# Optimization experiments

Measured on AMD Instinct MI355X. Metric: run time of the kernel, lower is better.

Reference implementation:

```python
import jax, jax.numpy as jnp
import numpy as np

N = 50000
E = 1000000
D_IN = 128
D_HID = 128
D_EMB = 128
D_DEG = 32
NEG_SLOPE = 0.2


def _add_self_loops(src, dst, n):
    loop = jnp.arange(n, dtype=src.dtype)
    return jnp.concatenate([src, loop]), jnp.concatenate([dst, loop])


def gat_conv(x, src, dst, W, a_src, a_dst, b, n):
    """PyG GATConv, heads=1, add_self_loops=True. src/dst already include self loops."""
    h = x @ W                                   # [n, d_out]
    hs = h[src]                                 # [e, d_out] gather (message sources)
    e = jax.nn.leaky_relu(hs @ a_src + h[dst] @ a_dst, NEG_SLOPE)  # [e]
    m = jax.ops.segment_max(e, dst, num_segments=n)
    e = jnp.exp(e - m[dst])
    denom = jax.ops.segment_sum(e, dst, num_segments=n)
    alpha = e / (denom[dst] + 1e-16)
    out = jax.ops.segment_sum(alpha[:, None] * hs, dst, num_segments=n)
    return out + b


def setup_inputs() -> dict:
    key = jax.random.key(0)
    ks = jax.random.split(key, 24)
    p = lambda k, shape: (jax.random.normal(k, shape, dtype=jnp.float32) * 0.05)
    inp = {
        "x_o": jax.random.normal(ks[0], (N, D_IN), dtype=jnp.float32),
        "degree_o": jax.random.normal(ks[1], (N, D_DEG), dtype=jnp.float32),
        "edge_index_o": jax.random.randint(ks[2], (2, E), 0, N, dtype=jnp.int32),
        "edge_index_s": jax.random.randint(ks[3], (2, E), 0, N, dtype=jnp.int32),
        # GAT layer params: o1, o2, s1, s2
        "W_o1": p(ks[4], (D_IN, D_HID)), "a_src_o1": p(ks[5], (D_HID,)), "a_dst_o1": p(ks[6], (D_HID,)), "b_o1": jnp.zeros((D_HID,), jnp.float32),
        "W_o2": p(ks[7], (D_HID, D_EMB)), "a_src_o2": p(ks[8], (D_EMB,)), "a_dst_o2": p(ks[9], (D_EMB,)), "b_o2": jnp.zeros((D_EMB,), jnp.float32),
        "W_s1": p(ks[10], (D_IN, D_HID)), "a_src_s1": p(ks[11], (D_HID,)), "a_dst_s1": p(ks[12], (D_HID,)), "b_s1": jnp.zeros((D_HID,), jnp.float32),
        "W_s2": p(ks[13], (D_HID, D_EMB)), "a_src_s2": p(ks[14], (D_EMB,)), "a_dst_s2": p(ks[15], (D_EMB,)), "b_s2": jnp.zeros((D_EMB,), jnp.float32),
        "W_pred": p(ks[16], (2 * D_EMB + D_DEG, 2)), "b_pred": jnp.zeros((2,), jnp.float32),
    }
    return inp


def reference(x_o, degree_o,
              W_o1, a_src_o1, a_dst_o1, b_o1,
              W_o2, a_src_o2, a_dst_o2, b_o2,
              W_s1, a_src_s1, a_dst_s1, b_s1,
              W_s2, a_src_s2, a_dst_s2, b_s2,
              W_pred, b_pred,
              edge_index_o, edge_index_s):
    n = x_o.shape[0]
    src_o, dst_o = _add_self_loops(edge_index_o[0], edge_index_o[1], n)
    src_s, dst_s = _add_self_loops(edge_index_s[0], edge_index_s[1], n)

    # branch o (original graph); dropout is identity in eval mode
    x1_o = jax.nn.relu(gat_conv(x_o, src_o, dst_o, W_o1, a_src_o1, a_dst_o1, b_o1, n))
    x2_o = gat_conv(x1_o, src_o, dst_o, W_o2, a_src_o2, a_dst_o2, b_o2, n)
    # branch s (second graph)
    x1_s = jax.nn.relu(gat_conv(x_o, src_s, dst_s, W_s1, a_src_s1, a_dst_s1, b_s1, n))
    x2_s = gat_conv(x1_s, src_s, dst_s, W_s2, a_src_s2, a_dst_s2, b_s2, n)

    x2_os = jnp.concatenate([x2_o, x2_s, degree_o], axis=1)   # [n, 2*emb+deg]
    attn = jax.nn.softmax(x2_os @ W_pred + b_pred, axis=1)    # [n, 2]
    pred = attn[:, :1] * x2_o + attn[:, 1:] * x2_s            # [n, emb]
    return pred
```

## Files before the change

kernel.cpp:

```cpp
#include <hip/hip_runtime.h>
#include <hip/hip_fp16.h>
#include <math.h>


#define LRELU(v) ((v) > 0.f ? (v) : 0.2f * (v))

#define BSHIFT 7
#define BSIZE  128
#define MAXB   512
#define CHUNK  4096
#define EPT    16
#define MAXE   4352
#define CAPI   (MAXE + BSIZE)
#define WTSZ   17408

typedef _Float16 half8 __attribute__((ext_vector_type(8)));
typedef float f32x4 __attribute__((ext_vector_type(4)));


__global__ void k_binit(int* bcur_o, int* bcur_s, int nbuck) {
    int i = blockIdx.x * 256 + threadIdx.x;
    if (i < nbuck) { bcur_o[i] = i * MAXE; bcur_s[i] = i * MAXE; }
}

__global__ __launch_bounds__(256) void k_bin_scatter(
    const int* __restrict__ src_o, const int* __restrict__ dst_o,
    const int* __restrict__ src_s, const int* __restrict__ dst_s,
    int* bcur_o, int* bcur_s, int* ebin_o, int* ebin_s, int E)
{
    __shared__ int cnt[MAXB];
    __shared__ int gb[MAXB];
    int t = threadIdx.x;
    int base = blockIdx.x * CHUNK;

    for (int g = 0; g < 2; g++) {
        const int* srcp = g ? src_s : src_o;
        const int* dstp = g ? dst_s : dst_o;
        int* bcur = g ? bcur_s : bcur_o;
        int* ebin = g ? ebin_s : ebin_o;
        for (int i = t; i < MAXB; i += 256) cnt[i] = 0;
        __syncthreads();
        int pk[EPT], bk[EPT], rk[EPT];
        #pragma unroll
        for (int j = 0; j < EPT; j++) {
            int e = base + j * 256 + t;
            bk[j] = -1; pk[j] = 0; rk[j] = 0;
            if (e < E) {
                int d = dstp[e];
                int s = srcp[e];
                int bb = d >> BSHIFT;
                bk[j] = bb;
                pk[j] = ((d & (BSIZE - 1)) << 16) | s;
                rk[j] = atomicAdd(&cnt[bb], 1);
            }
        }
        __syncthreads();
        for (int i = t; i < MAXB; i += 256) {
            int c = cnt[i];
            gb[i] = c ? atomicAdd(&bcur[i], c) : 0;
        }
        __syncthreads();
        #pragma unroll
        for (int j = 0; j < EPT; j++) {
            if (bk[j] >= 0) {
                int p = gb[bk[j]] + rk[j];
                if (p < (bk[j] + 1) * MAXE) ebin[p] = pk[j];
            }
        }
        __syncthreads();
    }
}

__global__ __launch_bounds__(256) void k_sort(
    const int* __restrict__ ebin_o, const int* __restrict__ bcur_o,
    int* __restrict__ off_o, int* __restrict__ dend_o, unsigned short* __restrict__ idx_o,
    const int* __restrict__ ebin_s, const int* __restrict__ bcur_s,
    int* __restrict__ off_s, int* __restrict__ dend_s, unsigned short* __restrict__ idx_s,
    int N)
{
    const int* ebin = blockIdx.y ? ebin_s : ebin_o;
    const int* bcur = blockIdx.y ? bcur_s : bcur_o;
    int* off  = blockIdx.y ? off_s  : off_o;
    int* dend = blockIdx.y ? dend_s : dend_o;
    unsigned short* idx = blockIdx.y ? idx_s : idx_o;

    __shared__ int pack[MAXE];
    __shared__ int sorted[MAXE + BSIZE];
    __shared__ int cnt[BSIZE + 1];
    __shared__ int s2[BSIZE + 1];
    __shared__ int noff[BSIZE + 1];

    int b = blockIdx.x;
    int t = threadIdx.x;
    int node0 = b << BSHIFT;
    int nloc = min(BSIZE, N - node0);
    int ebeg = b * MAXE;
    int ne = min(bcur[b] - ebeg, MAXE);
    int ib = b * CAPI;

    for (int i = t; i < ne; i += 256) pack[i] = ebin[ebeg + i];
    if (t < BSIZE + 1) cnt[t] = (t < nloc) ? 1 : 0;
    __syncthreads();
    for (int i = t; i < ne; i += 256) atomicAdd(&cnt[pack[i] >> 16], 1);
    __syncthreads();
    if (t < BSIZE + 1) s2[t] = cnt[t];
    __syncthreads();
    for (int d = 1; d <= BSIZE; d <<= 1) {
        int v = (t < BSIZE + 1 && t >= d) ? s2[t - d] : 0;
        __syncthreads();
        if (t < BSIZE + 1) s2[t] += v;
        __syncthreads();
    }
    if (t < BSIZE + 1) noff[t] = s2[t] - cnt[t];
    __syncthreads();
    if (t < nloc) {
        off[node0 + t]  = ib + noff[t];
        dend[node0 + t] = ib + s2[t];
        cnt[t] = noff[t] + 1;
        sorted[noff[t]] = node0 + t;
    }
    __syncthreads();
    for (int i = t; i < ne; i += 256) {
        int p = atomicAdd(&cnt[pack[i] >> 16], 1);
        sorted[p] = pack[i] & 0xffff;
    }
    __syncthreads();
    int tot = ne + nloc;
    for (int i = t; i < tot; i += 256) idx[ib + i] = (unsigned short)sorted[i];
}


__global__ __launch_bounds__(256) void k_prepw(
    const float* __restrict__ W0, const float* __restrict__ W1,
    const float* __restrict__ W2, const float* __restrict__ W3,
    _Float16* __restrict__ WtG)
{
    int i = blockIdx.x * 256 + threadIdx.x;
    int w = i >> 14;
    int rem = i & 16383;
    int nn = rem >> 7;
    int k = rem & 127;
    const float* W = (w == 0) ? W0 : (w == 1) ? W1 : (w == 2) ? W2 : W3;
    WtG[w * WTSZ + nn * 136 + k] = (_Float16)W[k * 128 + nn];
}


template<typename IT>
__global__ __launch_bounds__(256) void k_gemm2(
    const IT* __restrict__ X0, const IT* __restrict__ X1,
    const _Float16* __restrict__ WtA, const _Float16* __restrict__ WtB,
    const float* __restrict__ as0, const float* __restrict__ ad0,
    const float* __restrict__ as1, const float* __restrict__ ad1,
    __half* __restrict__ H0, __half* __restrict__ H1,
    float* __restrict__ S0, float* __restrict__ D0,
    float* __restrict__ S1, float* __restrict__ D1,
    int n)
{
    int br = blockIdx.y;
    const IT* X = br ? X1 : X0;
    const _Float16* WtGp = br ? WtB : WtA;
    const float* a_src = br ? as1 : as0;
    const float* a_dst = br ? ad1 : ad0;
    __half* H = br ? H1 : H0;
    float* Svec = br ? S1 : S0;
    float* Dvec = br ? D1 : D0;

    __shared__ _Float16 As[64 * 136];
    __shared__ _Float16 Wt[128 * 136];
    int tid = threadIdx.x;
    int m0 = blockIdx.x * 64;

    for (int i = tid; i < WTSZ / 8; i += 256)
        ((uint4*)Wt)[i] = ((const uint4*)WtGp)[i];
    if constexpr (sizeof(IT) == 4) {
        for (int i = tid; i < 64 * 32; i += 256) {
            int r = i >> 5;
            int c4 = (i & 31) << 2;
            int row = m0 + r; if (row >= n) row = n - 1;
            float4 v = *(const float4*)&X[(size_t)row * 128 + c4];
            _Float16* p = &As[r * 136 + c4];
            p[0] = (_Float16)v.x; p[1] = (_Float16)v.y;
            p[2] = (_Float16)v.z; p[3] = (_Float16)v.w;
        }
    } else {
        for (int i = tid; i < 64 * 16; i += 256) {
            int r = i >> 4;
            int c8 = (i & 15) << 3;
            int row = m0 + r; if (row >= n) row = n - 1;
            *(uint4*)&As[r * 136 + c8] =
                *(const uint4*)&X[(size_t)row * 128 + c8];
        }
    }
    __syncthreads();

    int wave = tid >> 6;
    int lane = tid & 63;
    int m = lane & 15;
    int q = lane >> 4;
    int arow = wave * 16 + m;

    f32x4 acc[8];
    #pragma unroll
    for (int nt = 0; nt < 8; nt++) acc[nt] = (f32x4){0.f, 0.f, 0.f, 0.f};

    #pragma unroll
    for (int k0 = 0; k0 < 128; k0 += 32) {
        half8 a = *(half8*)&As[arow * 136 + k0 + q * 8];
        #pragma unroll
        for (int nt = 0; nt < 8; nt++) {
            half8 b = *(half8*)&Wt[(nt * 16 + m) * 136 + k0 + q * 8];
            acc[nt] = __builtin_amdgcn_mfma_f32_16x16x32_f16(a, b, acc[nt], 0, 0, 0);
        }
    }

    float sp[4] = {0.f, 0.f, 0.f, 0.f};
    float dp[4] = {0.f, 0.f, 0.f, 0.f};
    #pragma unroll
    for (int nt = 0; nt < 8; nt++) {
        float asv = a_src[nt * 16 + m];
        float adv = a_dst[nt * 16 + m];
        #pragma unroll
        for (int r = 0; r < 4; r++) {
            sp[r] = fmaf(acc[nt][r], asv, sp[r]);
            dp[r] = fmaf(acc[nt][r], adv, dp[r]);
        }
    }
    #pragma unroll
    for (int msk = 1; msk < 16; msk <<= 1) {
        #pragma unroll
        for (int r = 0; r < 4; r++) {
            sp[r] += __shfl_xor(sp[r], msk);
            dp[r] += __shfl_xor(dp[r], msk);
        }
    }
    if (m == 0) {
        #pragma unroll
        for (int r = 0; r < 4; r++) {
            int row = m0 + wave * 16 + q * 4 + r;
            if (row < n) { Svec[row] = sp[r]; Dvec[row] = dp[r]; }
        }
    }

    #pragma unroll
    for (int nt = 0; nt < 8; nt++) {
        #pragma unroll
        for (int r = 0; r < 4; r++) {
            As[(wave * 16 + q * 4 + r) * 136 + nt * 16 + m] = (_Float16)acc[nt][r];
        }
    }
    __syncthreads();
    for (int i = tid; i < 1024; i += 256) {
        int r = i >> 4;
        int c8 = (i & 15) << 3;
        int row = m0 + r;
        if (row < n)
            *(uint4*)&H[(size_t)row * 128 + c8] = *(uint4*)&As[r * 136 + c8];
    }
}


template<typename OT>
__global__ __launch_bounds__(256) void k_agg2(
    const __half* __restrict__ H0, const __half* __restrict__ H1,
    const float* __restrict__ S0, const float* __restrict__ D0,
    const float* __restrict__ S1, const float* __restrict__ D1,
    const int* __restrict__ off0, const int* __restrict__ dend0,
    const unsigned short* __restrict__ idx0,
    const int* __restrict__ off1, const int* __restrict__ dend1,
    const unsigned short* __restrict__ idx1,
    const float* __restrict__ b0, const float* __restrict__ b1,
    OT* __restrict__ out0, OT* __restrict__ out1,
    int n, int do_relu)
{
    int br = blockIdx.y;
    const __half* H = br ? H1 : H0;
    const float* Svec = br ? S1 : S0;
    const float* Dvec = br ? D1 : D0;
    const int* off  = br ? off1  : off0;
    const int* dend = br ? dend1 : dend0;
    const unsigned short* idx = br ? idx1 : idx0;
    const float* bias = br ? b1 : b0;
    OT* out = br ? out1 : out0;

    int wave = threadIdx.x >> 6;
    int lane = threadIdx.x & 63;
    int node = blockIdx.x * 4 + wave;
    if (node >= n) return;

    int beg = off[node];
    int end = dend[node];
    float dn = Dvec[node];

    int q = lane >> 4;
    int subl = lane & 15;
    float acc[8];
    #pragma unroll
    for (int j = 0; j < 8; j++) acc[j] = 0.f;
    float denom = 0.f;

    for (int base = beg; base < end; base += 64) {
        int cnt = min(64, end - base);
        float w = 0.f;
        int s = 0;
        if (lane < cnt) {
            s = idx[base + lane];
            float v = Svec[s] + dn;
            w = __expf(LRELU(v));
        }
        denom += w;
        int cnt32 = (cnt + 31) & ~31;
        for (int kk = 0; kk < cnt32; kk += 32) {
            int k0 = kk + q;
            float w0 = __shfl(w, k0);
            float w1 = __shfl(w, k0 + 4);
            float w2 = __shfl(w, k0 + 8);
            float w3 = __shfl(w, k0 + 12);
            float w4 = __shfl(w, k0 + 16);
            float w5 = __shfl(w, k0 + 20);
            float w6 = __shfl(w, k0 + 24);
            float w7 = __shfl(w, k0 + 28);
            int s0 = __shfl(s, k0);
            int s1 = __shfl(s, k0 + 4);
            int s2 = __shfl(s, k0 + 8);
            int s3 = __shfl(s, k0 + 12);
            int s4 = __shfl(s, k0 + 16);
            int s5 = __shfl(s, k0 + 20);
            int s6 = __shfl(s, k0 + 24);
            int s7 = __shfl(s, k0 + 28);
            uint4 u0 = ((const uint4*)(H + (size_t)s0 * 128))[subl];
            uint4 u1 = ((const uint4*)(H + (size_t)s1 * 128))[subl];
            uint4 u2 = ((const uint4*)(H + (size_t)s2 * 128))[subl];
            uint4 u3 = ((const uint4*)(H + (size_t)s3 * 128))[subl];
            uint4 u4 = ((const uint4*)(H + (size_t)s4 * 128))[subl];
            uint4 u5 = ((const uint4*)(H + (size_t)s5 * 128))[subl];
            uint4 u6 = ((const uint4*)(H + (size_t)s6 * 128))[subl];
            uint4 u7 = ((const uint4*)(H + (size_t)s7 * 128))[subl];
            const _Float16* p;
            p = (const _Float16*)&u0;
            #pragma unroll
            for (int j = 0; j < 8; j++) acc[j] = fmaf((float)p[j], w0, acc[j]);
            p = (const _Float16*)&u1;
            #pragma unroll
            for (int j = 0; j < 8; j++) acc[j] = fmaf((float)p[j], w1, acc[j]);
            p = (const _Float16*)&u2;
            #pragma unroll
            for (int j = 0; j < 8; j++) acc[j] = fmaf((float)p[j], w2, acc[j]);
            p = (const _Float16*)&u3;
            #pragma unroll
            for (int j = 0; j < 8; j++) acc[j] = fmaf((float)p[j], w3, acc[j]);
            p = (const _Float16*)&u4;
            #pragma unroll
            for (int j = 0; j < 8; j++) acc[j] = fmaf((float)p[j], w4, acc[j]);
            p = (const _Float16*)&u5;
            #pragma unroll
            for (int j = 0; j < 8; j++) acc[j] = fmaf((float)p[j], w5, acc[j]);
            p = (const _Float16*)&u6;
            #pragma unroll
            for (int j = 0; j < 8; j++) acc[j] = fmaf((float)p[j], w6, acc[j]);
            p = (const _Float16*)&u7;
            #pragma unroll
            for (int j = 0; j < 8; j++) acc[j] = fmaf((float)p[j], w7, acc[j]);
        }
    }
    #pragma unroll
    for (int j = 0; j < 8; j++) {
        acc[j] += __shfl_xor(acc[j], 16);
        acc[j] += __shfl_xor(acc[j], 32);
    }
    #pragma unroll
    for (int o = 32; o; o >>= 1) denom += __shfl_xor(denom, o);

    if (q == 0) {
        float inv = 1.f / (denom + 1e-16f);
        int cb = subl << 3;
        float vals[8];
        #pragma unroll
        for (int j = 0; j < 8; j++) {
            float v = acc[j] * inv + bias[cb + j];
            if (do_relu) v = fmaxf(v, 0.f);
            vals[j] = v;
        }
        if constexpr (sizeof(OT) == 2) {
            half8 hv;
            #pragma unroll
            for (int j = 0; j < 8; j++) hv[j] = (_Float16)vals[j];
            *(half8*)&out[(size_t)node * 128 + cb] = hv;
        } else {
            float4 o0, o1;
            o0.x = vals[0]; o0.y = vals[1]; o0.z = vals[2]; o0.w = vals[3];
            o1.x = vals[4]; o1.y = vals[5]; o1.z = vals[6]; o1.w = vals[7];
            *(float4*)&out[(size_t)node * 128 + cb] = o0;
            *(float4*)&out[(size_t)node * 128 + cb + 4] = o1;
        }
    }
}


__global__ __launch_bounds__(256) void k_pred(
    const float* __restrict__ x2o, const float* __restrict__ x2s,
    const float* __restrict__ deg,
    const float* __restrict__ Wp, const float* __restrict__ bp,
    float* __restrict__ out, int n)
{
    int wave = threadIdx.x >> 6;
    int lane = threadIdx.x & 63;
    int node = blockIdx.x * 4 + wave;
    if (node >= n) return;

    float acc0 = 0.f, acc1 = 0.f;
    for (int i = lane; i < 288; i += 64) {
        float v;
        if (i < 128)      v = x2o[(size_t)node * 128 + i];
        else if (i < 256) v = x2s[(size_t)node * 128 + (i - 128)];
        else              v = deg[(size_t)node * 32 + (i - 256)];
        acc0 += v * Wp[i * 2];
        acc1 += v * Wp[i * 2 + 1];
    }
    for (int o = 32; o; o >>= 1) {
        acc0 += __shfl_xor(acc0, o);
        acc1 += __shfl_xor(acc1, o);
    }
    float z0 = acc0 + bp[0];
    float z1 = acc1 + bp[1];
    float mz = fmaxf(z0, z1);
    float e0 = __expf(z0 - mz);
    float e1 = __expf(z1 - mz);
    float a0 = e0 / (e0 + e1);
    float a1 = 1.f - a0;
    float2 vo = *(const float2*)&x2o[(size_t)node * 128 + 2 * lane];
    float2 vs = *(const float2*)&x2s[(size_t)node * 128 + 2 * lane];
    float2 r;
    r.x = a0 * vo.x + a1 * vs.x;
    r.y = a0 * vo.y + a1 * vs.y;
    *(float2*)&out[(size_t)node * 128 + 2 * lane] = r;
}


extern "C" void kernel_launch(void* const* d_in, const int* in_sizes, int n_in,
                              void* d_out, int out_size, void* d_ws, size_t ws_size,
                              hipStream_t stream) {
    const float* x_o    = (const float*)d_in[0];
    const float* degree = (const float*)d_in[1];
    const int*   ei_o   = (const int*)d_in[2];
    const int*   ei_s   = (const int*)d_in[3];
    const float* W_o1 = (const float*)d_in[4];
    const float* asr_o1 = (const float*)d_in[5];
    const float* ads_o1 = (const float*)d_in[6];
    const float* b_o1 = (const float*)d_in[7];
    const float* W_o2 = (const float*)d_in[8];
    const float* asr_o2 = (const float*)d_in[9];
    const float* ads_o2 = (const float*)d_in[10];
    const float* b_o2 = (const float*)d_in[11];
    const float* W_s1 = (const float*)d_in[12];
    const float* asr_s1 = (const float*)d_in[13];
    const float* ads_s1 = (const float*)d_in[14];
    const float* b_s1 = (const float*)d_in[15];
    const float* W_s2 = (const float*)d_in[16];
    const float* asr_s2 = (const float*)d_in[17];
    const float* ads_s2 = (const float*)d_in[18];
    const float* b_s2 = (const float*)d_in[19];
    const float* W_pred = (const float*)d_in[20];
    const float* b_pred = (const float*)d_in[21];
    float* out = (float*)d_out;

    const int N = in_sizes[0] / 128;
    const int E = in_sizes[2] / 2;
    const int NBUCK = (N + BSIZE - 1) >> BSHIFT;

    char* ws = (char*)d_ws;
    size_t o = 0;
    auto alloc = [&](size_t bytes) -> char* {
        char* p = ws + o;
        o += (bytes + 255) & ~(size_t)255;
        return p;
    };
    int* bcur_o = (int*)alloc((size_t)NBUCK * 4);
    int* bcur_s = (int*)alloc((size_t)NBUCK * 4);
    int* off_o  = (int*)alloc((size_t)N * 4);
    int* dend_o = (int*)alloc((size_t)N * 4);
    int* off_s  = (int*)alloc((size_t)N * 4);
    int* dend_s = (int*)alloc((size_t)N * 4);
    unsigned short* idx_o = (unsigned short*)alloc((size_t)NBUCK * CAPI * 2);
    unsigned short* idx_s = (unsigned short*)alloc((size_t)NBUCK * CAPI * 2);
    _Float16* WtG = (_Float16*)alloc((size_t)4 * WTSZ * 2);
    float* Sv_o = (float*)alloc((size_t)N * 4);
    float* Dv_o = (float*)alloc((size_t)N * 4);
    float* Sv_s = (float*)alloc((size_t)N * 4);
    float* Dv_s = (float*)alloc((size_t)N * 4);
    __half* h_o   = (__half*)alloc((size_t)N * 128 * 2);
    __half* h_s   = (__half*)alloc((size_t)N * 128 * 2);
    __half* x1h_o = (__half*)alloc((size_t)N * 128 * 2);
    __half* x1h_s = (__half*)alloc((size_t)N * 128 * 2);
    float* B1 = (float*)alloc((size_t)N * 128 * 4);
    float* B2 = (float*)alloc((size_t)N * 128 * 4);
    (void)ws_size;

    int* ebin_o = (int*)B1;
    int* ebin_s = (int*)B1 + (size_t)NBUCK * MAXE;

    dim3 blk(256);
    int gBin  = (E + CHUNK - 1) / CHUNK;
    int gGemm = (N + 63) / 64;
    int gNode = (N + 3) / 4;

    k_binit<<<(NBUCK + 255) / 256, blk, 0, stream>>>(bcur_o, bcur_s, NBUCK);
    k_prepw<<<256, blk, 0, stream>>>(W_o1, W_o2, W_s1, W_s2, WtG);
    k_bin_scatter<<<gBin, blk, 0, stream>>>(ei_o, ei_o + E, ei_s, ei_s + E,
                                            bcur_o, bcur_s, ebin_o, ebin_s, E);
    dim3 gSort(NBUCK, 2);
    k_sort<<<gSort, blk, 0, stream>>>(ebin_o, bcur_o, off_o, dend_o, idx_o,
                                      ebin_s, bcur_s, off_s, dend_s, idx_s, N);

    dim3 gG(gGemm, 2), gA(gNode, 2);
    k_gemm2<float><<<gG, blk, 0, stream>>>(
        x_o, x_o, WtG, WtG + 2 * WTSZ,
        asr_o1, ads_o1, asr_s1, ads_s1,
        h_o, h_s, Sv_o, Dv_o, Sv_s, Dv_s, N);
    k_agg2<__half><<<gA, blk, 0, stream>>>(
        h_o, h_s, Sv_o, Dv_o, Sv_s, Dv_s,
        off_o, dend_o, idx_o, off_s, dend_s, idx_s,
        b_o1, b_s1, x1h_o, x1h_s, N, 1);
    k_gemm2<__half><<<gG, blk, 0, stream>>>(
        x1h_o, x1h_s, WtG + WTSZ, WtG + 3 * WTSZ,
        asr_o2, ads_o2, asr_s2, ads_s2,
        h_o, h_s, Sv_o, Dv_o, Sv_s, Dv_s, N);
    k_agg2<float><<<gA, blk, 0, stream>>>(
        h_o, h_s, Sv_o, Dv_o, Sv_s, Dv_s,
        off_o, dend_o, idx_o, off_s, dend_s, idx_s,
        b_o2, b_s2, B1, B2, N, 0);

    k_pred<<<gNode, blk, 0, stream>>>(B1, B2, degree, W_pred, b_pred, out, N);
}
```

Before: 399.7 us.

## Fuse second-layer aggregation with prediction and pack fp16 weights with indices

The second aggregation now processes both branches per node inside one kernel and applies the prediction softmax blend directly. This removes the fp32 intermediate buffers and the separate k_pred pass. The edge weight is rounded to fp16 and packed with the 16-bit source index into a single int, which halves the shuffles per edge. The inner loop is also cut from 8 to 4 loads per step. The edge-binning scratch buffer is remapped onto the h_o/h_s buffers. Risks: the fused grid has half as many blocks, the loop has less memory-level parallelism, and fp16 rounding of weights adds error.

```diff
diff --git a/kernel.cpp b/kernel.cpp
--- a/kernel.cpp
+++ b/kernel.cpp
@@ -259,82 +259,40 @@
 }
 
 
-template<typename OT>
-__global__ __launch_bounds__(256) void k_agg2(
-    const __half* __restrict__ H0, const __half* __restrict__ H1,
-    const float* __restrict__ S0, const float* __restrict__ D0,
-    const float* __restrict__ S1, const float* __restrict__ D1,
-    const int* __restrict__ off0, const int* __restrict__ dend0,
-    const unsigned short* __restrict__ idx0,
-    const int* __restrict__ off1, const int* __restrict__ dend1,
-    const unsigned short* __restrict__ idx1,
-    const float* __restrict__ b0, const float* __restrict__ b1,
-    OT* __restrict__ out0, OT* __restrict__ out1,
-    int n, int do_relu)
-{
-    int br = blockIdx.y;
-    const __half* H = br ? H1 : H0;
-    const float* Svec = br ? S1 : S0;
-    const float* Dvec = br ? D1 : D0;
-    const int* off  = br ? off1  : off0;
-    const int* dend = br ? dend1 : dend0;
-    const unsigned short* idx = br ? idx1 : idx0;
-    const float* bias = br ? b1 : b0;
-    OT* out = br ? out1 : out0;
-
-    int wave = threadIdx.x >> 6;
-    int lane = threadIdx.x & 63;
-    int node = blockIdx.x * 4 + wave;
-    if (node >= n) return;
-
-    int beg = off[node];
-    int end = dend[node];
-    float dn = Dvec[node];
-
-    int q = lane >> 4;
-    int subl = lane & 15;
-    float acc[8];
+__device__ __forceinline__ void agg_core(
+    const __half* __restrict__ H, const float* __restrict__ Svec, float dn,
+    const unsigned short* __restrict__ idx, int beg, int end,
+    int lane, int q, int subl, float* acc, float& denom)
+{
     #pragma unroll
     for (int j = 0; j < 8; j++) acc[j] = 0.f;
-    float denom = 0.f;
-
+    denom = 0.f;
     for (int base = beg; base < end; base += 64) {
         int cnt = min(64, end - base);
-        float w = 0.f;
-        int s = 0;
+        int pk = 0;
         if (lane < cnt) {
-            s = idx[base + lane];
+            int s = idx[base + lane];
             float v = Svec[s] + dn;
-            w = __expf(LRELU(v));
-        }
-        denom += w;
-        int cnt32 = (cnt + 31) & ~31;
-        for (int kk = 0; kk < cnt32; kk += 32) {
+            float w = __expf(LRELU(v));
+            _Float16 wh = (_Float16)w;
+            denom += (float)wh;
+            pk = ((int)__builtin_bit_cast(unsigned short, wh) << 16) | s;
+        }
+        int cnt16 = (cnt + 15) & ~15;
+        for (int kk = 0; kk < cnt16; kk += 16) {
             int k0 = kk + q;
-            float w0 = __shfl(w, k0);
-            float w1 = __shfl(w, k0 + 4);
-            float w2 = __shfl(w, k0 + 8);
-            float w3 = __shfl(w, k0 + 12);
-            float w4 = __shfl(w, k0 + 16);
-            float w5 = __shfl(w, k0 + 20);
-            float w6 = __shfl(w, k0 + 24);
-            float w7 = __shfl(w, k0 + 28);
-            int s0 = __shfl(s, k0);
-            int s1 = __shfl(s, k0 + 4);
-            int s2 = __shfl(s, k0 + 8);
-            int s3 = __shfl(s, k0 + 12);
-            int s4 = __shfl(s, k0 + 16);
-            int s5 = __shfl(s, k0 + 20);
-            int s6 = __shfl(s, k0 + 24);
-            int s7 = __shfl(s, k0 + 28);
-            uint4 u0 = ((const uint4*)(H + (size_t)s0 * 128))[subl];
-            uint4 u1 = ((const uint4*)(H + (size_t)s1 * 128))[subl];
-            uint4 u2 = ((const uint4*)(H + (size_t)s2 * 128))[subl];
-            uint4 u3 = ((const uint4*)(H + (size_t)s3 * 128))[subl];
-            uint4 u4 = ((const uint4*)(H + (size_t)s4 * 128))[subl];
-            uint4 u5 = ((const uint4*)(H + (size_t)s5 * 128))[subl];
-            uint4 u6 = ((const uint4*)(H + (size_t)s6 * 128))[subl];
-            uint4 u7 = ((const uint4*)(H + (size_t)s7 * 128))[subl];
+            int p0 = __shfl(pk, k0);
+            int p1 = __shfl(pk, k0 + 4);
+            int p2 = __shfl(pk, k0 + 8);
+            int p3 = __shfl(pk, k0 + 12);
+            uint4 u0 = ((const uint4*)(H + (size_t)(p0 & 0xffff) * 128))[subl];
+            uint4 u1 = ((const uint4*)(H + (size_t)(p1 & 0xffff) * 128))[subl];
+            uint4 u2 = ((const uint4*)(H + (size_t)(p2 & 0xffff) * 128))[subl];
+            uint4 u3 = ((const uint4*)(H + (size_t)(p3 & 0xffff) * 128))[subl];
+            float w0 = (float)__builtin_bit_cast(_Float16, (unsigned short)(p0 >> 16));
+            float w1 = (float)__builtin_bit_cast(_Float16, (unsigned short)(p1 >> 16));
+            float w2 = (float)__builtin_bit_cast(_Float16, (unsigned short)(p2 >> 16));
+            float w3 = (float)__builtin_bit_cast(_Float16, (unsigned short)(p3 >> 16));
             const _Float16* p;
             p = (const _Float16*)&u0;
             #pragma unroll
@@ -348,18 +306,6 @@
             p = (const _Float16*)&u3;
             #pragma unroll
             for (int j = 0; j < 8; j++) acc[j] = fmaf((float)p[j], w3, acc[j]);
-            p = (const _Float16*)&u4;
-            #pragma unroll
-            for (int j = 0; j < 8; j++) acc[j] = fmaf((float)p[j], w4, acc[j]);
-            p = (const _Float16*)&u5;
-            #pragma unroll
-            for (int j = 0; j < 8; j++) acc[j] = fmaf((float)p[j], w5, acc[j]);
-            p = (const _Float16*)&u6;
-            #pragma unroll
-            for (int j = 0; j < 8; j++) acc[j] = fmaf((float)p[j], w6, acc[j]);
-            p = (const _Float16*)&u7;
-            #pragma unroll
-            for (int j = 0; j < 8; j++) acc[j] = fmaf((float)p[j], w7, acc[j]);
         }
     }
     #pragma unroll
@@ -369,70 +315,135 @@
     }
     #pragma unroll
     for (int o = 32; o; o >>= 1) denom += __shfl_xor(denom, o);
-
-    if (q == 0) {
-        float inv = 1.f / (denom + 1e-16f);
-        int cb = subl << 3;
-        float vals[8];
-        #pragma unroll
-        for (int j = 0; j < 8; j++) {
-            float v = acc[j] * inv + bias[cb + j];
-            if (do_relu) v = fmaxf(v, 0.f);
-            vals[j] = v;
-        }
-        if constexpr (sizeof(OT) == 2) {
-            half8 hv;
-            #pragma unroll
-            for (int j = 0; j < 8; j++) hv[j] = (_Float16)vals[j];
-            *(half8*)&out[(size_t)node * 128 + cb] = hv;
-        } else {
-            float4 o0, o1;
-            o0.x = vals[0]; o0.y = vals[1]; o0.z = vals[2]; o0.w = vals[3];
-            o1.x = vals[4]; o1.y = vals[5]; o1.z = vals[6]; o1.w = vals[7];
-            *(float4*)&out[(size_t)node * 128 + cb] = o0;
-            *(float4*)&out[(size_t)node * 128 + cb + 4] = o1;
-        }
-    }
-}
-
-
-__global__ __launch_bounds__(256) void k_pred(
-    const float* __restrict__ x2o, const float* __restrict__ x2s,
-    const float* __restrict__ deg,
-    const float* __restrict__ Wp, const float* __restrict__ bp,
-    float* __restrict__ out, int n)
-{
+}
+
+
+__global__ __launch_bounds__(256) void k_agg1(
+    const __half* __restrict__ H0, const __half* __restrict__ H1,
+    const float* __restrict__ S0, const float* __restrict__ D0,
+    const float* __restrict__ S1, const float* __restrict__ D1,
+    const int* __restrict__ off0, const int* __restrict__ dend0,
+    const unsigned short* __restrict__ idx0,
+    const int* __restrict__ off1, const int* __restrict__ dend1,
+    const unsigned short* __restrict__ idx1,
+    const float* __restrict__ b0, const float* __restrict__ b1,
+    __half* __restrict__ out0, __half* __restrict__ out1,
+    int n)
+{
+    int br = blockIdx.y;
+    const __half* H = br ? H1 : H0;
+    const float* Svec = br ? S1 : S0;
+    const float* Dvec = br ? D1 : D0;
+    const int* off  = br ? off1  : off0;
+    const int* dend = br ? dend1 : dend0;
+    const unsigned short* idx = br ? idx1 : idx0;
+    const float* bias = br ? b1 : b0;
+    __half* out = br ? out1 : out0;
+
     int wave = threadIdx.x >> 6;
     int lane = threadIdx.x & 63;
     int node = blockIdx.x * 4 + wave;
     if (node >= n) return;
 
-    float acc0 = 0.f, acc1 = 0.f;
-    for (int i = lane; i < 288; i += 64) {
-        float v;
-        if (i < 128)      v = x2o[(size_t)node * 128 + i];
-        else if (i < 256) v = x2s[(size_t)node * 128 + (i - 128)];
-        else              v = deg[(size_t)node * 32 + (i - 256)];
-        acc0 += v * Wp[i * 2];
-        acc1 += v * Wp[i * 2 + 1];
-    }
-    for (int o = 32; o; o >>= 1) {
-        acc0 += __shfl_xor(acc0, o);
-        acc1 += __shfl_xor(acc1, o);
-    }
-    float z0 = acc0 + bp[0];
-    float z1 = acc1 + bp[1];
-    float mz = fmaxf(z0, z1);
-    float e0 = __expf(z0 - mz);
-    float e1 = __expf(z1 - mz);
-    float a0 = e0 / (e0 + e1);
-    float a1 = 1.f - a0;
-    float2 vo = *(const float2*)&x2o[(size_t)node * 128 + 2 * lane];
-    float2 vs = *(const float2*)&x2s[(size_t)node * 128 + 2 * lane];
-    float2 r;
-    r.x = a0 * vo.x + a1 * vs.x;
-    r.y = a0 * vo.y + a1 * vs.y;
-    *(float2*)&out[(size_t)node * 128 + 2 * lane] = r;
+    int q = lane >> 4;
+    int subl = lane & 15;
+    float acc[8], denom;
+    agg_core(H, Svec, Dvec[node], idx, off[node], dend[node],
+             lane, q, subl, acc, denom);
+
+    if (q == 0) {
+        float inv = 1.f / (denom + 1e-16f);
+        int cb = subl << 3;
+        half8 hv;
+        #pragma unroll
+        for (int j = 0; j < 8; j++) {
+            float v = fmaxf(acc[j] * inv + bias[cb + j], 0.f);
+            hv[j] = (_Float16)v;
+        }
+        *(half8*)&out[(size_t)node * 128 + cb] = hv;
+    }
+}
+
+
+__global__ __launch_bounds__(256) void k_agg_pred(
+    const __half* __restrict__ H0, const __half* __restrict__ H1,
+    const float* __restrict__ S0, const float* __restrict__ D0,
+    const float* __restrict__ S1, const float* __restrict__ D1,
+    const int* __restrict__ off0, const int* __restrict__ dend0,
+    const unsigned short* __restrict__ idx0,
+    const int* __restrict__ off1, const int* __restrict__ dend1,
+    const unsigned short* __restrict__ idx1,
+    const float* __restrict__ b0, const float* __restrict__ b1,
+    const float* __restrict__ deg,
+    const float* __restrict__ Wp, const float* __restrict__ bp,
+    float* __restrict__ out, int n)
+{
+    int wave = threadIdx.x >> 6;
+    int lane = threadIdx.x & 63;
+    int node = blockIdx.x * 4 + wave;
+    if (node >= n) return;
+
+    int q = lane >> 4;
+    int subl = lane & 15;
+    int cb = subl << 3;
+
+    float acc[8], denom;
+    float vo[8], vs[8];
+
+    agg_core(H0, S0, D0[node], idx0, off0[node], dend0[node],
+             lane, q, subl, acc, denom);
+    {
+        float inv = 1.f / (denom + 1e-16f);
+        #pragma unroll
+        for (int j = 0; j < 8; j++) vo[j] = acc[j] * inv + b0[cb + j];
+    }
+    agg_core(H1, S1, D1[node], idx1, off1[node], dend1[node],
+             lane, q, subl, acc, denom);
+    {
+        float inv = 1.f / (denom + 1e-16f);
+        #pragma unroll
+        for (int j = 0; j < 8; j++) vs[j] = acc[j] * inv + b1[cb + j];
+    }
+
+    if (q == 0) {
+        float z0 = 0.f, z1 = 0.f;
+        #pragma unroll
+        for (int j = 0; j < 8; j++) {
+            int c = cb + j;
+            z0 = fmaf(vo[j], Wp[c * 2],     z0);
+            z1 = fmaf(vo[j], Wp[c * 2 + 1], z1);
+            z0 = fmaf(vs[j], Wp[(128 + c) * 2],     z0);
+            z1 = fmaf(vs[j], Wp[(128 + c) * 2 + 1], z1);
+        }
+        float2 dv = *(const float2*)&deg[(size_t)node * 32 + 2 * subl];
+        z0 = fmaf(dv.x, Wp[(256 + 2 * subl) * 2],     z0);
+        z1 = fmaf(dv.x, Wp[(256 + 2 * subl) * 2 + 1], z1);
+        z0 = fmaf(dv.y, Wp[(257 + 2 * subl) * 2],     z0);
+        z1 = fmaf(dv.y, Wp[(257 + 2 * subl) * 2 + 1], z1);
+        #pragma unroll
+        for (int msk = 1; msk < 16; msk <<= 1) {
+            z0 += __shfl_xor(z0, msk);
+            z1 += __shfl_xor(z1, msk);
+        }
+        z0 += bp[0];
+        z1 += bp[1];
+        float mz = fmaxf(z0, z1);
+        float e0 = __expf(z0 - mz);
+        float e1 = __expf(z1 - mz);
+        float a0 = e0 / (e0 + e1);
+        float a1 = 1.f - a0;
+        float4 r0, r1;
+        r0.x = a0 * vo[0] + a1 * vs[0];
+        r0.y = a0 * vo[1] + a1 * vs[1];
+        r0.z = a0 * vo[2] + a1 * vs[2];
+        r0.w = a0 * vo[3] + a1 * vs[3];
+        r1.x = a0 * vo[4] + a1 * vs[4];
+        r1.y = a0 * vo[5] + a1 * vs[5];
+        r1.z = a0 * vo[6] + a1 * vs[6];
+        r1.w = a0 * vo[7] + a1 * vs[7];
+        *(float4*)&out[(size_t)node * 128 + cb] = r0;
+        *(float4*)&out[(size_t)node * 128 + cb + 4] = r1;
+    }
 }
 
 
@@ -491,12 +502,10 @@
     __half* h_s   = (__half*)alloc((size_t)N * 128 * 2);
     __half* x1h_o = (__half*)alloc((size_t)N * 128 * 2);
     __half* x1h_s = (__half*)alloc((size_t)N * 128 * 2);
-    float* B1 = (float*)alloc((size_t)N * 128 * 4);
-    float* B2 = (float*)alloc((size_t)N * 128 * 4);
     (void)ws_size;
 
-    int* ebin_o = (int*)B1;
-    int* ebin_s = (int*)B1 + (size_t)NBUCK * MAXE;
+    int* ebin_o = (int*)h_o;
+    int* ebin_s = (int*)h_s;
 
     dim3 blk(256);
     int gBin  = (E + CHUNK - 1) / CHUNK;
@@ -516,18 +525,16 @@
         x_o, x_o, WtG, WtG + 2 * WTSZ,
         asr_o1, ads_o1, asr_s1, ads_s1,
         h_o, h_s, Sv_o, Dv_o, Sv_s, Dv_s, N);
-    k_agg2<__half><<<gA, blk, 0, stream>>>(
+    k_agg1<<<gA, blk, 0, stream>>>(
         h_o, h_s, Sv_o, Dv_o, Sv_s, Dv_s,
         off_o, dend_o, idx_o, off_s, dend_s, idx_s,
-        b_o1, b_s1, x1h_o, x1h_s, N, 1);
+        b_o1, b_s1, x1h_o, x1h_s, N);
     k_gemm2<__half><<<gG, blk, 0, stream>>>(
         x1h_o, x1h_s, WtG + WTSZ, WtG + 3 * WTSZ,
         asr_o2, ads_o2, asr_s2, ads_s2,
         h_o, h_s, Sv_o, Dv_o, Sv_s, Dv_s, N);
-    k_agg2<float><<<gA, blk, 0, stream>>>(
+    k_agg_pred<<<gNode, blk, 0, stream>>>(
         h_o, h_s, Sv_o, Dv_o, Sv_s, Dv_s,
         off_o, dend_o, idx_o, off_s, dend_s, idx_s,
-        b_o2, b_s2, B1, B2, N, 0);
-
-    k_pred<<<gNode, blk, 0, stream>>>(B1, B2, degree, W_pred, b_pred, out, N);
-}
+        b_o2, b_s2, degree, W_pred, b_pred, out, N);
+}
```

Result: faster. 364.2 us (-8.9%).
